# Kernel tuning notes

Measured on AMD Instinct MI355X. Metric: run time of the kernel, lower is better.

The kernel has to match this reference:

```python
import jax, jax.numpy as jnp
import numpy as np

EMB = 1024  # embedding_size in the torch module


def setup_inputs() -> dict:
    key = jax.random.key(0)
    ks = jax.random.split(key, 6)
    B, N, K = 64, 256, 4096
    y = jax.random.normal(ks[0], (B, N, 1024), dtype=jnp.float32)
    # nn.Linear weights, init normal(std=0.02), zero bias
    Wy_w = jax.random.normal(ks[1], (1024, 1024), dtype=jnp.float32) * 0.02  # [out,in]
    Wy_b = jnp.zeros((1024,), dtype=jnp.float32)
    Wz_w = jax.random.normal(ks[2], (1024, 2048), dtype=jnp.float32) * 0.02  # [out,in]
    Wz_b = jnp.zeros((1024,), dtype=jnp.float32)
    dic_z = jax.random.normal(ks[3], (K, 2048), dtype=jnp.float32)
    prior = jax.random.uniform(ks[4], (K,), dtype=jnp.float32)
    prior = prior / jnp.sum(prior)
    return {"y": y, "Wy_w": Wy_w, "Wy_b": Wy_b, "Wz_w": Wz_w, "Wz_b": Wz_b,
            "dic_z": dic_z, "prior": prior}


def reference(y, Wy_w, Wy_b, Wz_w, Wz_b, dic_z, prior):
    # h = Wy(y): [B,N,1024]; dz = Wz(dic_z): [K,1024]
    h = jnp.einsum('bni,oi->bno', y, Wy_w) + Wy_b
    dz = jnp.einsum('ki,oi->ko', dic_z, Wz_w) + Wz_b
    # attention over dictionary: [B,N,K]
    att = jax.nn.softmax(jnp.einsum('bnd,kd->bnk', h, dz) / jnp.sqrt(jnp.float32(EMB)), axis=-1)
    # z[b,n] = sum_k prior[k] * att[b,n,k] * dic_z[k]  -> [B,N,2048]
    # (avoids the [B,N,K,2048] intermediate the torch code materializes)
    z = jnp.einsum('bnk,k,ke->bne', att, prior, dic_z)
    return z
```

## Files before the change

kernel.cpp:

```cpp
#include <hip/hip_runtime.h>
#include <hip/hip_bf16.h>
#include <stdint.h>

typedef __bf16 bf16;
typedef __bf16 bf16x4 __attribute__((ext_vector_type(4)));
typedef __bf16 bf16x8 __attribute__((ext_vector_type(8)));
typedef float f32x4 __attribute__((ext_vector_type(4)));
typedef unsigned short ushort8 __attribute__((ext_vector_type(8)));

__device__ __forceinline__ void gload16(const bf16* g, char* l) {
  __builtin_amdgcn_global_load_lds(
      reinterpret_cast<const __attribute__((address_space(1))) unsigned int*>(
          reinterpret_cast<uintptr_t>(g)),
      reinterpret_cast<__attribute__((address_space(3))) unsigned int*>(
          reinterpret_cast<uintptr_t>(l)),
      16, 0, 0);
}

#define VMCNT(n)  asm volatile("s_waitcnt vmcnt(" #n ")" ::: "memory")
#define LGKM0()   do { asm volatile("s_waitcnt lgkmcnt(0)" ::: "memory"); \
                       __builtin_amdgcn_sched_barrier(0); } while (0)
#define BAR()     __builtin_amdgcn_s_barrier()

__global__ __launch_bounds__(256) void cast_bf16(const float* __restrict__ in,
                                                 bf16* __restrict__ out, int n8) {
  int i = blockIdx.x * blockDim.x + threadIdx.x;
  const int stride = gridDim.x * blockDim.x;
  for (; i < n8; i += stride) {
    const float4 v0 = reinterpret_cast<const float4*>(in)[i * 2];
    const float4 v1 = reinterpret_cast<const float4*>(in)[i * 2 + 1];
    bf16x8 o = { (bf16)v0.x, (bf16)v0.y, (bf16)v0.z, (bf16)v0.w,
                 (bf16)v1.x, (bf16)v1.y, (bf16)v1.z, (bf16)v1.w };
    reinterpret_cast<bf16x8*>(out)[i] = o;
  }
}

__global__ __launch_bounds__(256) void rowsum_bf16(const unsigned short* __restrict__ S,
                                                   float* __restrict__ sums) {
  const int row = blockIdx.x * 4 + (threadIdx.x >> 6);
  const int lane = threadIdx.x & 63;
  const unsigned short* r = S + (size_t)row * 4096;
  float s = 0.f;
#pragma unroll
  for (int i = 0; i < 8; ++i) {
    ushort8 v = *reinterpret_cast<const ushort8*>(r + i * 512 + lane * 8);
#pragma unroll
    for (int j = 0; j < 8; ++j) s += __uint_as_float(((unsigned)v[j]) << 16);
  }
#pragma unroll
  for (int o = 32; o; o >>= 1) s += __shfl_xor(s, o);
  if (lane == 0) sums[row] = s;
}

template <int EPI, int BN>
__global__ __launch_bounds__(512, 2) void gemm8(
    const bf16* __restrict__ A, const bf16* __restrict__ B,
    const float* __restrict__ aux, void* __restrict__ Cout,
    int M, int N, int K, float scale) {
  constexpr int BUFSZ = 32768 + BN * 128;
  constexpr int BOFF = 32768;
  constexpr int TM = (BN == 256) ? 128 : 64;
  constexpr int MI = TM / 16;
  constexpr int NI = 4;
  extern __shared__ char lds[];
  const int tid = threadIdx.x;
  const int lane = tid & 63, w = tid >> 6;

  const int gridN = N / BN;
  const int nwg = gridDim.x;
  const int orig = blockIdx.x;
  int wgid;
  { const int q = nwg >> 3, r = nwg & 7, x = orig & 7, rest = orig >> 3;
    wgid = (x < r ? x * (q + 1) : r * (q + 1) + (x - r) * q) + rest; }
  const int m0 = (wgid / gridN) * 256;
  const int n0 = (wgid % gridN) * BN;

  const int srow = lane >> 3;
  const int scol = ((lane & 7) ^ srow) * 8;
  const bf16* gA = A + (size_t)(m0 + w * 8 + srow) * K + scol;
  const bf16* gB = B + (size_t)(n0 + w * 8 + srow) * K + scol;

  auto stA = [&](char* dst, int u, int h) {
    gload16(gA + (size_t)(h * 128) * K + (size_t)u * 64, dst + h * 16384 + w * 1024);
    gload16(gA + (size_t)(h * 128 + 64) * K + (size_t)u * 64, dst + h * 16384 + 8192 + w * 1024);
  };
  auto stB = [&](char* dst, int u, int h) {
    gload16(gB + (size_t)(h * 128) * K + (size_t)u * 64, dst + BOFF + h * 16384 + w * 1024);
    gload16(gB + (size_t)(h * 128 + 64) * K + (size_t)u * 64, dst + BOFF + h * 16384 + 8192 + w * 1024);
  };

  const int fr = lane & 15, hi = lane >> 4;
  int wm, wn;
  if constexpr (BN == 256) { wm = w >> 2; wn = w & 3; }
  else                     { wm = w >> 1; wn = w & 1; }
  const int abase = (wm * TM + fr) * 128 + ((hi ^ (fr & 7)) << 4);
  const int bbase = BOFF + (wn * 64 + fr) * 128 + ((hi ^ (fr & 7)) << 4);
#define RD_A(b, mi, ks) (*(const bf16x8*)((b) + ((abase + (mi) * 2048) ^ ((ks) << 6))))
#define RD_B(b, ni, ks) (*(const bf16x8*)((b) + ((bbase + (ni) * 2048) ^ ((ks) << 6))))

  f32x4 acc[MI][NI] = {};
  const int NT = K >> 6;

  stA(lds, 0, 0); stA(lds, 0, 1);
  stB(lds, 0, 0);
  if constexpr (BN == 256) stB(lds, 0, 1);
  stB(lds + BUFSZ, 1, 0);
  if constexpr (BN == 256) { stB(lds + BUFSZ, 1, 1); VMCNT(4); }
  else                     { VMCNT(2); }
  BAR();

  for (int u = 0; u < NT; ++u) {
    char* b  = lds + (size_t)(u & 1) * BUFSZ;
    char* bn = lds + (size_t)((u + 1) & 1) * BUFSZ;
    bf16x8 bb[2][NI], a[2][2];
    const bool sA = (u + 1) < NT, sB = (u + 2) < NT;

    if constexpr (BN == 256) {
      a[0][0] = RD_A(b, 0, 0); a[0][1] = RD_A(b, 0, 1);
      a[1][0] = RD_A(b, 1, 0); a[1][1] = RD_A(b, 1, 1);
#pragma unroll
      for (int ni = 0; ni < NI; ++ni) { bb[0][ni] = RD_B(b, ni, 0); bb[1][ni] = RD_B(b, ni, 1); }
      if (sA) stA(bn, u + 1, 0);
      BAR(); LGKM0();
      __builtin_amdgcn_s_setprio(1);
#pragma unroll
      for (int m2 = 0; m2 < 2; ++m2)
#pragma unroll
        for (int ni = 0; ni < NI; ++ni) {
          acc[m2][ni] = __builtin_amdgcn_mfma_f32_16x16x32_bf16(a[m2][0], bb[0][ni], acc[m2][ni], 0, 0, 0);
          acc[m2][ni] = __builtin_amdgcn_mfma_f32_16x16x32_bf16(a[m2][1], bb[1][ni], acc[m2][ni], 0, 0, 0);
        }
      __builtin_amdgcn_s_setprio(0);
      BAR();
      a[0][0] = RD_A(b, 2, 0); a[0][1] = RD_A(b, 2, 1);
      a[1][0] = RD_A(b, 3, 0); a[1][1] = RD_A(b, 3, 1);
      if (sA) stA(bn, u + 1, 1);
      BAR(); LGKM0();
      __builtin_amdgcn_s_setprio(1);
#pragma unroll
      for (int m2 = 0; m2 < 2; ++m2)
#pragma unroll
        for (int ni = 0; ni < NI; ++ni) {
          acc[2 + m2][ni] = __builtin_amdgcn_mfma_f32_16x16x32_bf16(a[m2][0], bb[0][ni], acc[2 + m2][ni], 0, 0, 0);
          acc[2 + m2][ni] = __builtin_amdgcn_mfma_f32_16x16x32_bf16(a[m2][1], bb[1][ni], acc[2 + m2][ni], 0, 0, 0);
        }
      __builtin_amdgcn_s_setprio(0);
      BAR();
      a[0][0] = RD_A(b, 4, 0); a[0][1] = RD_A(b, 4, 1);
      a[1][0] = RD_A(b, 5, 0); a[1][1] = RD_A(b, 5, 1);
      if (sB) stB(b, u + 2, 0);
      BAR(); LGKM0();
      __builtin_amdgcn_s_setprio(1);
#pragma unroll
      for (int m2 = 0; m2 < 2; ++m2)
#pragma unroll
        for (int ni = 0; ni < NI; ++ni) {
          acc[4 + m2][ni] = __builtin_amdgcn_mfma_f32_16x16x32_bf16(a[m2][0], bb[0][ni], acc[4 + m2][ni], 0, 0, 0);
          acc[4 + m2][ni] = __builtin_amdgcn_mfma_f32_16x16x32_bf16(a[m2][1], bb[1][ni], acc[4 + m2][ni], 0, 0, 0);
        }
      __builtin_amdgcn_s_setprio(0);
      BAR();
      a[0][0] = RD_A(b, 6, 0); a[0][1] = RD_A(b, 6, 1);
      a[1][0] = RD_A(b, 7, 0); a[1][1] = RD_A(b, 7, 1);
      if (sB) stB(b, u + 2, 1);
      BAR(); LGKM0();
      __builtin_amdgcn_s_setprio(1);
#pragma unroll
      for (int m2 = 0; m2 < 2; ++m2)
#pragma unroll
        for (int ni = 0; ni < NI; ++ni) {
          acc[6 + m2][ni] = __builtin_amdgcn_mfma_f32_16x16x32_bf16(a[m2][0], bb[0][ni], acc[6 + m2][ni], 0, 0, 0);
          acc[6 + m2][ni] = __builtin_amdgcn_mfma_f32_16x16x32_bf16(a[m2][1], bb[1][ni], acc[6 + m2][ni], 0, 0, 0);
        }
      __builtin_amdgcn_s_setprio(0);
      if (sB) VMCNT(4); else VMCNT(0);
      BAR();
    } else {
      a[0][0] = RD_A(b, 0, 0); a[0][1] = RD_A(b, 0, 1);
      a[1][0] = RD_A(b, 1, 0); a[1][1] = RD_A(b, 1, 1);
#pragma unroll
      for (int ni = 0; ni < NI; ++ni) { bb[0][ni] = RD_B(b, ni, 0); bb[1][ni] = RD_B(b, ni, 1); }
      if (sA) { stA(bn, u + 1, 0); stA(bn, u + 1, 1); }
      BAR(); LGKM0();
      __builtin_amdgcn_s_setprio(1);
#pragma unroll
      for (int m2 = 0; m2 < 2; ++m2)
#pragma unroll
        for (int ni = 0; ni < NI; ++ni) {
          acc[m2][ni] = __builtin_amdgcn_mfma_f32_16x16x32_bf16(a[m2][0], bb[0][ni], acc[m2][ni], 0, 0, 0);
          acc[m2][ni] = __builtin_amdgcn_mfma_f32_16x16x32_bf16(a[m2][1], bb[1][ni], acc[m2][ni], 0, 0, 0);
        }
      __builtin_amdgcn_s_setprio(0);
      BAR();
      a[0][0] = RD_A(b, 2, 0); a[0][1] = RD_A(b, 2, 1);
      a[1][0] = RD_A(b, 3, 0); a[1][1] = RD_A(b, 3, 1);
      if (sB) stB(b, u + 2, 0);
      BAR(); LGKM0();
      __builtin_amdgcn_s_setprio(1);
#pragma unroll
      for (int m2 = 0; m2 < 2; ++m2)
#pragma unroll
        for (int ni = 0; ni < NI; ++ni) {
          acc[2 + m2][ni] = __builtin_amdgcn_mfma_f32_16x16x32_bf16(a[m2][0], bb[0][ni], acc[2 + m2][ni], 0, 0, 0);
          acc[2 + m2][ni] = __builtin_amdgcn_mfma_f32_16x16x32_bf16(a[m2][1], bb[1][ni], acc[2 + m2][ni], 0, 0, 0);
        }
      __builtin_amdgcn_s_setprio(0);
      if (sB) VMCNT(2); else VMCNT(0);
      BAR();
    }
  }
#undef RD_A
#undef RD_B

  float* lsum = (float*)lds;
  if constexpr (EPI == 2) {
    if (tid < 256) lsum[tid] = aux[m0 + tid];
    __syncthreads();
  }

  const int lro = hi * 4;
  if constexpr (EPI == 2) {
#pragma unroll
    for (int mi = 0; mi < MI; ++mi)
#pragma unroll
      for (int j = 0; j < 4; ++j) {
        const int lr = wm * TM + mi * 16 + lro + j;
        const float inv = 1.0f / lsum[lr];
        const size_t grow = (size_t)(m0 + lr) * N;
#pragma unroll
        for (int ni = 0; ni < NI; ++ni)
          ((float*)Cout)[grow + n0 + wn * 64 + ni * 16 + fr] = acc[mi][ni][j] * inv;
      }
  } else {
#pragma unroll
    for (int ni = 0; ni < NI; ++ni) {
      const int gcol = n0 + wn * 64 + ni * 16 + fr;
      float bvs = 0.f;
      if constexpr (EPI == 0) bvs = aux[gcol];
#pragma unroll
      for (int mi = 0; mi < MI; ++mi) {
        const int grow = m0 + wm * TM + mi * 16 + lro;
#pragma unroll
        for (int j = 0; j < 4; ++j) {
          float c = acc[mi][ni][j] * scale + bvs;
          if constexpr (EPI == 1) c = __expf(c);
          ((bf16*)Cout)[(size_t)(grow + j) * N + gcol] = (bf16)c;
        }
      }
    }
  }
}

__global__ __launch_bounds__(256) void prep_dic(const float* __restrict__ dic,
                                                const float* __restrict__ prior,
                                                bf16* __restrict__ dicb,
                                                bf16* __restrict__ w3t) {
  const int KD = 4096, E = 2048;
  __shared__ bf16 t[64][72];
  const int k0 = blockIdx.x * 64, e0 = blockIdx.y * 64;
  const int tid = threadIdx.x;
  const int er = (tid & 15) * 4;
  const int kr = tid >> 4;
#pragma unroll
  for (int p = 0; p < 4; ++p) {
    const int k = kr + p * 16;
    const float pr = prior[k0 + k];
    const float4 v = *reinterpret_cast<const float4*>(dic + (size_t)(k0 + k) * E + e0 + er);
    bf16x4 db = { (bf16)v.x, (bf16)v.y, (bf16)v.z, (bf16)v.w };
    *reinterpret_cast<bf16x4*>(dicb + (size_t)(k0 + k) * E + e0 + er) = db;
    t[er + 0][k] = (bf16)(v.x * pr);
    t[er + 1][k] = (bf16)(v.y * pr);
    t[er + 2][k] = (bf16)(v.z * pr);
    t[er + 3][k] = (bf16)(v.w * pr);
  }
  __syncthreads();
  const int e = tid >> 2, kc = (tid & 3) * 16;
  ushort8 a = *reinterpret_cast<ushort8*>(&t[e][kc]);
  ushort8 b = *reinterpret_cast<ushort8*>(&t[e][kc + 8]);
  unsigned short* dst = (unsigned short*)w3t + (size_t)(e0 + e) * KD + k0 + kc;
  *reinterpret_cast<ushort8*>(dst) = a;
  *reinterpret_cast<ushort8*>(dst + 8) = b;
}

extern "C" void kernel_launch(void* const* d_in, const int* in_sizes, int n_in,
                              void* d_out, int out_size, void* d_ws, size_t ws_size,
                              hipStream_t stream) {
  const float* y     = (const float*)d_in[0];
  const float* Wy_w  = (const float*)d_in[1];
  const float* Wy_b  = (const float*)d_in[2];
  const float* Wz_w  = (const float*)d_in[3];
  const float* Wz_b  = (const float*)d_in[4];
  const float* dic   = (const float*)d_in[5];
  const float* prior = (const float*)d_in[6];
  float* z = (float*)d_out;

  const int M = 16384, D = 1024, E = 2048, KD = 4096;

  char* ws = (char*)d_ws;
  bf16* w3t  = (bf16*)(ws);
  bf16* h    = (bf16*)(ws + ((size_t)16 << 20));
  bf16* dzb  = (bf16*)(ws + ((size_t)48 << 20));
  bf16* S    = (bf16*)(ws + ((size_t)56 << 20));
  bf16* yb   = (bf16*)(ws + ((size_t)56 << 20));
  bf16* Wyb  = (bf16*)(ws + ((size_t)88 << 20));
  bf16* Wzb  = (bf16*)(ws + ((size_t)90 << 20));
  bf16* dicb = (bf16*)(ws + ((size_t)94 << 20));
  float* sums = (float*)(ws + ((size_t)16 << 20));

  cast_bf16<<<2048, 256, 0, stream>>>(y, yb, M * D / 8);
  cast_bf16<<<512, 256, 0, stream>>>(Wy_w, Wyb, D * D / 8);
  cast_bf16<<<512, 256, 0, stream>>>(Wz_w, Wzb, D * E / 8);
  prep_dic<<<dim3(KD / 64, E / 64), 256, 0, stream>>>(dic, prior, dicb, w3t);
  gemm8<0, 256><<<(M / 256) * (D / 256), 512, 131072, stream>>>(
      yb, Wyb, Wy_b, h, M, D, D, 1.0f);
  gemm8<0, 128><<<(KD / 256) * (D / 128), 512, 98304, stream>>>(
      dicb, Wzb, Wz_b, dzb, KD, D, E, 1.0f);
  gemm8<1, 256><<<(M / 256) * (KD / 256), 512, 131072, stream>>>(
      h, dzb, nullptr, S, M, KD, D, 0.03125f);
  rowsum_bf16<<<M / 4, 256, 0, stream>>>((const unsigned short*)S, sums);
  gemm8<2, 256><<<(M / 256) * (E / 256), 512, 131072, stream>>>(
      S, w3t, sums, z, M, E, KD, 1.0f);
}
```

Baseline: 538.3 us.

## Switch GEMM inner loop to 32x32x16 MFMA with two-phase pipeline

Replaces the 16x16x32 bf16 MFMA tiling with 32x32x16 MFMA, so each wave holds 32x32 accumulator tiles and issues fewer, larger matrix instructions with fewer LDS fragment reads per FLOP. The loop is restructured from four or two sub-phases per K-step into two phases, each staging a whole A or B tile with merged global-to-LDS loads. The epilogue is rewritten for the 32x32 output lane layout. This trades higher register pressure and larger fragment buffers for better MFMA efficiency and less LDS traffic.

```diff
diff --git a/kernel.cpp b/kernel.cpp
--- a/kernel.cpp
+++ b/kernel.cpp
@@ -5,7 +5,7 @@
 typedef __bf16 bf16;
 typedef __bf16 bf16x4 __attribute__((ext_vector_type(4)));
 typedef __bf16 bf16x8 __attribute__((ext_vector_type(8)));
-typedef float f32x4 __attribute__((ext_vector_type(4)));
+typedef float f32x16 __attribute__((ext_vector_type(16)));
 typedef unsigned short ushort8 __attribute__((ext_vector_type(8)));
 
 __device__ __forceinline__ void gload16(const bf16* g, char* l) {
@@ -60,8 +60,8 @@
   constexpr int BUFSZ = 32768 + BN * 128;
   constexpr int BOFF = 32768;
   constexpr int TM = (BN == 256) ? 128 : 64;
-  constexpr int MI = TM / 16;
-  constexpr int NI = 4;
+  constexpr int TI = TM / 32;
+  constexpr int TH = TI / 2;
   extern __shared__ char lds[];
   const int tid = threadIdx.x;
   const int lane = tid & 63, w = tid >> 6;
@@ -80,134 +80,93 @@
   const bf16* gA = A + (size_t)(m0 + w * 8 + srow) * K + scol;
   const bf16* gB = B + (size_t)(n0 + w * 8 + srow) * K + scol;
 
-  auto stA = [&](char* dst, int u, int h) {
-    gload16(gA + (size_t)(h * 128) * K + (size_t)u * 64, dst + h * 16384 + w * 1024);
-    gload16(gA + (size_t)(h * 128 + 64) * K + (size_t)u * 64, dst + h * 16384 + 8192 + w * 1024);
+  auto stA = [&](char* dst, int u) {
+    const size_t kc = (size_t)u * 64;
+    gload16(gA + kc, dst + w * 1024);
+    gload16(gA + (size_t)64 * K + kc, dst + 8192 + w * 1024);
+    gload16(gA + (size_t)128 * K + kc, dst + 16384 + w * 1024);
+    gload16(gA + (size_t)192 * K + kc, dst + 24576 + w * 1024);
   };
-  auto stB = [&](char* dst, int u, int h) {
-    gload16(gB + (size_t)(h * 128) * K + (size_t)u * 64, dst + BOFF + h * 16384 + w * 1024);
-    gload16(gB + (size_t)(h * 128 + 64) * K + (size_t)u * 64, dst + BOFF + h * 16384 + 8192 + w * 1024);
+  auto stB = [&](char* dst, int u) {
+    const size_t kc = (size_t)u * 64;
+    gload16(gB + kc, dst + BOFF + w * 1024);
+    gload16(gB + (size_t)64 * K + kc, dst + BOFF + 8192 + w * 1024);
+    if constexpr (BN == 256) {
+      gload16(gB + (size_t)128 * K + kc, dst + BOFF + 16384 + w * 1024);
+      gload16(gB + (size_t)192 * K + kc, dst + BOFF + 24576 + w * 1024);
+    }
   };
 
-  const int fr = lane & 15, hi = lane >> 4;
+  const int fq = lane & 31;
+  const int fh = lane >> 5;
   int wm, wn;
   if constexpr (BN == 256) { wm = w >> 2; wn = w & 3; }
   else                     { wm = w >> 1; wn = w & 1; }
-  const int abase = (wm * TM + fr) * 128 + ((hi ^ (fr & 7)) << 4);
-  const int bbase = BOFF + (wn * 64 + fr) * 128 + ((hi ^ (fr & 7)) << 4);
-#define RD_A(b, mi, ks) (*(const bf16x8*)((b) + ((abase + (mi) * 2048) ^ ((ks) << 6))))
-#define RD_B(b, ni, ks) (*(const bf16x8*)((b) + ((bbase + (ni) * 2048) ^ ((ks) << 6))))
-
-  f32x4 acc[MI][NI] = {};
+  const int arow = wm * TM + fq;
+  const int abase = arow * 128;
+  const int asw = arow & 7;
+  const int brow = wn * 64 + fq;
+  const int bbase = BOFF + brow * 128;
+  const int bsw = brow & 7;
+#define RD_A(b, ti, ks) (*(const bf16x8*)((b) + abase + (ti) * 4096 + ((((ks) * 2 + fh) ^ asw) << 4)))
+#define RD_B(b, ni, ks) (*(const bf16x8*)((b) + bbase + (ni) * 4096 + ((((ks) * 2 + fh) ^ bsw) << 4)))
+
+  f32x16 acc[TI][2] = {};
   const int NT = K >> 6;
 
-  stA(lds, 0, 0); stA(lds, 0, 1);
-  stB(lds, 0, 0);
-  if constexpr (BN == 256) stB(lds, 0, 1);
-  stB(lds + BUFSZ, 1, 0);
-  if constexpr (BN == 256) { stB(lds + BUFSZ, 1, 1); VMCNT(4); }
-  else                     { VMCNT(2); }
+  stA(lds, 0);
+  stB(lds, 0);
+  stB(lds + BUFSZ, 1);
+  if constexpr (BN == 256) VMCNT(4); else VMCNT(2);
   BAR();
 
   for (int u = 0; u < NT; ++u) {
-    char* b  = lds + (size_t)(u & 1) * BUFSZ;
-    char* bn = lds + (size_t)((u + 1) & 1) * BUFSZ;
-    bf16x8 bb[2][NI], a[2][2];
+    char* bcur = lds + (size_t)(u & 1) * BUFSZ;
+    char* bnx  = lds + (size_t)((u + 1) & 1) * BUFSZ;
     const bool sA = (u + 1) < NT, sB = (u + 2) < NT;
-
-    if constexpr (BN == 256) {
-      a[0][0] = RD_A(b, 0, 0); a[0][1] = RD_A(b, 0, 1);
-      a[1][0] = RD_A(b, 1, 0); a[1][1] = RD_A(b, 1, 1);
-#pragma unroll
-      for (int ni = 0; ni < NI; ++ni) { bb[0][ni] = RD_B(b, ni, 0); bb[1][ni] = RD_B(b, ni, 1); }
-      if (sA) stA(bn, u + 1, 0);
-      BAR(); LGKM0();
-      __builtin_amdgcn_s_setprio(1);
-#pragma unroll
-      for (int m2 = 0; m2 < 2; ++m2)
-#pragma unroll
-        for (int ni = 0; ni < NI; ++ni) {
-          acc[m2][ni] = __builtin_amdgcn_mfma_f32_16x16x32_bf16(a[m2][0], bb[0][ni], acc[m2][ni], 0, 0, 0);
-          acc[m2][ni] = __builtin_amdgcn_mfma_f32_16x16x32_bf16(a[m2][1], bb[1][ni], acc[m2][ni], 0, 0, 0);
-        }
-      __builtin_amdgcn_s_setprio(0);
-      BAR();
-      a[0][0] = RD_A(b, 2, 0); a[0][1] = RD_A(b, 2, 1);
-      a[1][0] = RD_A(b, 3, 0); a[1][1] = RD_A(b, 3, 1);
-      if (sA) stA(bn, u + 1, 1);
-      BAR(); LGKM0();
-      __builtin_amdgcn_s_setprio(1);
-#pragma unroll
-      for (int m2 = 0; m2 < 2; ++m2)
-#pragma unroll
-        for (int ni = 0; ni < NI; ++ni) {
-          acc[2 + m2][ni] = __builtin_amdgcn_mfma_f32_16x16x32_bf16(a[m2][0], bb[0][ni], acc[2 + m2][ni], 0, 0, 0);
-          acc[2 + m2][ni] = __builtin_amdgcn_mfma_f32_16x16x32_bf16(a[m2][1], bb[1][ni], acc[2 + m2][ni], 0, 0, 0);
-        }
-      __builtin_amdgcn_s_setprio(0);
-      BAR();
-      a[0][0] = RD_A(b, 4, 0); a[0][1] = RD_A(b, 4, 1);
-      a[1][0] = RD_A(b, 5, 0); a[1][1] = RD_A(b, 5, 1);
-      if (sB) stB(b, u + 2, 0);
-      BAR(); LGKM0();
-      __builtin_amdgcn_s_setprio(1);
-#pragma unroll
-      for (int m2 = 0; m2 < 2; ++m2)
-#pragma unroll
-        for (int ni = 0; ni < NI; ++ni) {
-          acc[4 + m2][ni] = __builtin_amdgcn_mfma_f32_16x16x32_bf16(a[m2][0], bb[0][ni], acc[4 + m2][ni], 0, 0, 0);
-          acc[4 + m2][ni] = __builtin_amdgcn_mfma_f32_16x16x32_bf16(a[m2][1], bb[1][ni], acc[4 + m2][ni], 0, 0, 0);
-        }
-      __builtin_amdgcn_s_setprio(0);
-      BAR();
-      a[0][0] = RD_A(b, 6, 0); a[0][1] = RD_A(b, 6, 1);
-      a[1][0] = RD_A(b, 7, 0); a[1][1] = RD_A(b, 7, 1);
-      if (sB) stB(b, u + 2, 1);
-      BAR(); LGKM0();
-      __builtin_amdgcn_s_setprio(1);
-#pragma unroll
-      for (int m2 = 0; m2 < 2; ++m2)
-#pragma unroll
-        for (int ni = 0; ni < NI; ++ni) {
-          acc[6 + m2][ni] = __builtin_amdgcn_mfma_f32_16x16x32_bf16(a[m2][0], bb[0][ni], acc[6 + m2][ni], 0, 0, 0);
-          acc[6 + m2][ni] = __builtin_amdgcn_mfma_f32_16x16x32_bf16(a[m2][1], bb[1][ni], acc[6 + m2][ni], 0, 0, 0);
-        }
-      __builtin_amdgcn_s_setprio(0);
-      if (sB) VMCNT(4); else VMCNT(0);
-      BAR();
-    } else {
-      a[0][0] = RD_A(b, 0, 0); a[0][1] = RD_A(b, 0, 1);
-      a[1][0] = RD_A(b, 1, 0); a[1][1] = RD_A(b, 1, 1);
-#pragma unroll
-      for (int ni = 0; ni < NI; ++ni) { bb[0][ni] = RD_B(b, ni, 0); bb[1][ni] = RD_B(b, ni, 1); }
-      if (sA) { stA(bn, u + 1, 0); stA(bn, u + 1, 1); }
-      BAR(); LGKM0();
-      __builtin_amdgcn_s_setprio(1);
-#pragma unroll
-      for (int m2 = 0; m2 < 2; ++m2)
-#pragma unroll
-        for (int ni = 0; ni < NI; ++ni) {
-          acc[m2][ni] = __builtin_amdgcn_mfma_f32_16x16x32_bf16(a[m2][0], bb[0][ni], acc[m2][ni], 0, 0, 0);
-          acc[m2][ni] = __builtin_amdgcn_mfma_f32_16x16x32_bf16(a[m2][1], bb[1][ni], acc[m2][ni], 0, 0, 0);
-        }
-      __builtin_amdgcn_s_setprio(0);
-      BAR();
-      a[0][0] = RD_A(b, 2, 0); a[0][1] = RD_A(b, 2, 1);
-      a[1][0] = RD_A(b, 3, 0); a[1][1] = RD_A(b, 3, 1);
-      if (sB) stB(b, u + 2, 0);
-      BAR(); LGKM0();
-      __builtin_amdgcn_s_setprio(1);
-#pragma unroll
-      for (int m2 = 0; m2 < 2; ++m2)
-#pragma unroll
-        for (int ni = 0; ni < NI; ++ni) {
-          acc[2 + m2][ni] = __builtin_amdgcn_mfma_f32_16x16x32_bf16(a[m2][0], bb[0][ni], acc[2 + m2][ni], 0, 0, 0);
-          acc[2 + m2][ni] = __builtin_amdgcn_mfma_f32_16x16x32_bf16(a[m2][1], bb[1][ni], acc[2 + m2][ni], 0, 0, 0);
-        }
-      __builtin_amdgcn_s_setprio(0);
-      if (sB) VMCNT(2); else VMCNT(0);
-      BAR();
-    }
+    bf16x8 bb[2][4], aq[TH][4];
+
+#pragma unroll
+    for (int ni = 0; ni < 2; ++ni)
+#pragma unroll
+      for (int ks = 0; ks < 4; ++ks) bb[ni][ks] = RD_B(bcur, ni, ks);
+#pragma unroll
+    for (int ti = 0; ti < TH; ++ti)
+#pragma unroll
+      for (int ks = 0; ks < 4; ++ks) aq[ti][ks] = RD_A(bcur, ti, ks);
+    if (sA) stA(bnx, u + 1);
+    BAR(); LGKM0();
+    __builtin_amdgcn_s_setprio(1);
+#pragma unroll
+    for (int ks = 0; ks < 4; ++ks)
+#pragma unroll
+      for (int ti = 0; ti < TH; ++ti)
+#pragma unroll
+        for (int ni = 0; ni < 2; ++ni)
+          acc[ti][ni] = __builtin_amdgcn_mfma_f32_32x32x16_bf16(
+              aq[ti][ks], bb[ni][ks], acc[ti][ni], 0, 0, 0);
+    __builtin_amdgcn_s_setprio(0);
+    BAR();
+
+#pragma unroll
+    for (int ti = 0; ti < TH; ++ti)
+#pragma unroll
+      for (int ks = 0; ks < 4; ++ks) aq[ti][ks] = RD_A(bcur, TH + ti, ks);
+    if (sB) stB(bcur, u + 2);
+    BAR(); LGKM0();
+    __builtin_amdgcn_s_setprio(1);
+#pragma unroll
+    for (int ks = 0; ks < 4; ++ks)
+#pragma unroll
+      for (int ti = 0; ti < TH; ++ti)
+#pragma unroll
+        for (int ni = 0; ni < 2; ++ni)
+          acc[TH + ti][ni] = __builtin_amdgcn_mfma_f32_32x32x16_bf16(
+              aq[ti][ks], bb[ni][ks], acc[TH + ti][ni], 0, 0, 0);
+    __builtin_amdgcn_s_setprio(0);
+    if (sB) { if constexpr (BN == 256) VMCNT(4); else VMCNT(2); }
+    else VMCNT(0);
+    BAR();
   }
 #undef RD_A
 #undef RD_B
@@ -218,33 +177,35 @@
     __syncthreads();
   }
 
-  const int lro = hi * 4;
   if constexpr (EPI == 2) {
 #pragma unroll
-    for (int mi = 0; mi < MI; ++mi)
-#pragma unroll
-      for (int j = 0; j < 4; ++j) {
-        const int lr = wm * TM + mi * 16 + lro + j;
+    for (int ti = 0; ti < TI; ++ti) {
+      const int rowb = wm * TM + ti * 32 + 4 * fh;
+#pragma unroll
+      for (int r = 0; r < 16; ++r) {
+        const int lr = rowb + (r & 3) + 8 * (r >> 2);
         const float inv = 1.0f / lsum[lr];
         const size_t grow = (size_t)(m0 + lr) * N;
 #pragma unroll
-        for (int ni = 0; ni < NI; ++ni)
-          ((float*)Cout)[grow + n0 + wn * 64 + ni * 16 + fr] = acc[mi][ni][j] * inv;
+        for (int ni = 0; ni < 2; ++ni)
+          ((float*)Cout)[grow + n0 + wn * 64 + ni * 32 + fq] = acc[ti][ni][r] * inv;
       }
+    }
   } else {
 #pragma unroll
-    for (int ni = 0; ni < NI; ++ni) {
-      const int gcol = n0 + wn * 64 + ni * 16 + fr;
+    for (int ni = 0; ni < 2; ++ni) {
+      const int gcol = n0 + wn * 64 + ni * 32 + fq;
       float bvs = 0.f;
       if constexpr (EPI == 0) bvs = aux[gcol];
 #pragma unroll
-      for (int mi = 0; mi < MI; ++mi) {
-        const int grow = m0 + wm * TM + mi * 16 + lro;
-#pragma unroll
-        for (int j = 0; j < 4; ++j) {
-          float c = acc[mi][ni][j] * scale + bvs;
+      for (int ti = 0; ti < TI; ++ti) {
+        const int rowb = m0 + wm * TM + ti * 32 + 4 * fh;
+#pragma unroll
+        for (int r = 0; r < 16; ++r) {
+          const int grow = rowb + (r & 3) + 8 * (r >> 2);
+          float c = acc[ti][ni][r] * scale + bvs;
           if constexpr (EPI == 1) c = __expf(c);
-          ((bf16*)Cout)[(size_t)(grow + j) * N + gcol] = (bf16)c;
+          ((bf16*)Cout)[(size_t)grow * N + gcol] = (bf16)c;
         }
       }
     }
```

After: 572.8 us. +6.4%, slower.
